# Optimization experiments

Measured on AMD Instinct MI355X. Metric: run time of the kernel, lower is better.

Reference implementation:

```python
import jax, jax.numpy as jnp
import numpy as np

D_MODEL = 768
D_STATE = 16
D_CONV = 4
EXPAND = 2
D_IN = D_MODEL // 2          # per-direction model dim = 384
D_INNER = EXPAND * D_IN      # ssm inner dim = 768
DT_RANK = (D_IN + 15) // 16  # 24 (mamba 'auto')
B, L = 2, 2048
EPS = 1e-5


def silu(x):
    return x * jax.nn.sigmoid(x)


def layernorm(x, w, b):
    m = jnp.mean(x, axis=-1, keepdims=True)
    v = jnp.var(x, axis=-1, keepdims=True)
    return (x - m) * jax.lax.rsqrt(v + EPS) * w + b


def causal_conv1d(u, w, b):
    # u: (B,L,di), w: (di,K) depthwise causal conv, b: (di,)
    K = w.shape[1]
    up = jnp.pad(u, ((0, 0), (K - 1, 0), (0, 0)))
    Lq = u.shape[1]
    y = sum(up[:, k:k + Lq, :] * w[:, k] for k in range(K))
    return y + b


def mamba_ssm(u, in_w, in_b, conv_w, conv_b, xp_w, dt_w, dt_b, A_log, Dp, out_w, out_b):
    # u: (B,L,D_IN)
    Bz = u.shape[0]
    xz = u @ in_w + in_b                         # (B,L,2*D_INNER)
    x, z = jnp.split(xz, 2, axis=-1)             # (B,L,D_INNER) each
    x = silu(causal_conv1d(x, conv_w, conv_b))
    xd = x @ xp_w                                # (B,L,DT_RANK+2N)
    dt = jax.nn.softplus(xd[..., :DT_RANK] @ dt_w + dt_b)   # (B,L,D_INNER)
    Bm = xd[..., DT_RANK:DT_RANK + D_STATE]      # (B,L,N)
    Cm = xd[..., DT_RANK + D_STATE:]             # (B,L,N)
    A = -jnp.exp(A_log)                          # (D_INNER,N)

    def step(h, xs):
        dt_t, x_t, B_t, C_t = xs                 # (B,di),(B,di),(B,N),(B,N)
        h = jnp.exp(dt_t[..., None] * A) * h + (dt_t * x_t)[..., None] * B_t[:, None, :]
        y = jnp.einsum('bdn,bn->bd', h, C_t)
        return h, y

    h0 = jnp.zeros((Bz, D_INNER, D_STATE), x.dtype)
    xs = (dt.transpose(1, 0, 2), x.transpose(1, 0, 2),
          Bm.transpose(1, 0, 2), Cm.transpose(1, 0, 2))
    _, ys = jax.lax.scan(step, h0, xs)           # ys: (L,B,D_INNER)
    y = ys.transpose(1, 0, 2) + x * Dp
    y = y * silu(z)
    return y @ out_w + out_b                     # (B,L,D_IN)


def setup_inputs() -> dict:
    key = jax.random.key(0)

    def nrm(i, shape, s=0.02):
        return jax.random.normal(jax.random.fold_in(key, i), shape, jnp.float32) * s

    d = {"x": jax.random.normal(jax.random.fold_in(key, 0), (B, L, D_MODEL), jnp.float32)}
    d["in_norm_w"] = jnp.ones(D_MODEL); d["in_norm_b"] = jnp.zeros(D_MODEL)
    d["ip_w"] = nrm(1, (D_MODEL, 2 * D_IN)); d["ip_b"] = jnp.zeros(2 * D_IN)
    i = 10
    for p in ("f", "b"):
        d[p + "_in_w"] = nrm(i, (D_IN, 2 * D_INNER)); d[p + "_in_b"] = jnp.zeros(2 * D_INNER)
        d[p + "_conv_w"] = nrm(i + 1, (D_INNER, D_CONV), 0.2); d[p + "_conv_b"] = jnp.zeros(D_INNER)
        d[p + "_xp_w"] = nrm(i + 2, (D_INNER, DT_RANK + 2 * D_STATE))
        d[p + "_dt_w"] = nrm(i + 3, (DT_RANK, D_INNER), 0.1)
        d[p + "_dt_b"] = nrm(i + 4, (D_INNER,), 0.5)
        d[p + "_A_log"] = jnp.log(jnp.tile(jnp.arange(1, D_STATE + 1, dtype=jnp.float32), (D_INNER, 1)))
        d[p + "_D"] = jnp.ones(D_INNER)
        d[p + "_out_w"] = nrm(i + 5, (D_INNER, D_IN)); d[p + "_out_b"] = jnp.zeros(D_IN)
        i += 10
    d["op_w"] = nrm(30, (2 * D_IN, D_MODEL)); d["op_b"] = jnp.zeros(D_MODEL)
    d["norm_w"] = jnp.ones(D_MODEL); d["norm_b"] = jnp.zeros(D_MODEL)
    return d


def reference(x, in_norm_w, in_norm_b, ip_w, ip_b,
              f_in_w, f_in_b, f_conv_w, f_conv_b, f_xp_w, f_dt_w, f_dt_b, f_A_log, f_D, f_out_w, f_out_b,
              b_in_w, b_in_b, b_conv_w, b_conv_b, b_xp_w, b_dt_w, b_dt_b, b_A_log, b_D, b_out_w, b_out_b,
              op_w, op_b, norm_w, norm_b):
    residual = x
    xn = layernorm(x, in_norm_w, in_norm_b)
    xp = xn @ ip_w + ip_b                        # (B,L,2*D_IN)
    x_fwd, x_bwd = jnp.split(xp, 2, axis=-1)
    out_fwd = mamba_ssm(x_fwd, f_in_w, f_in_b, f_conv_w, f_conv_b, f_xp_w,
                        f_dt_w, f_dt_b, f_A_log, f_D, f_out_w, f_out_b)
    out_bwd = mamba_ssm(jnp.flip(x_bwd, axis=1), b_in_w, b_in_b, b_conv_w, b_conv_b, b_xp_w,
                        b_dt_w, b_dt_b, b_A_log, b_D, b_out_w, b_out_b)
    out_bwd = jnp.flip(out_bwd, axis=1)
    out = jnp.concatenate([out_fwd, out_bwd], axis=-1) @ op_w + op_b
    # dropout is identity in eval mode
    return layernorm(residual + out, norm_w, norm_b)
```

## Files before the change

kernel.cpp:

```cpp
#include <hip/hip_runtime.h>
#include <hip/hip_bf16.h>
#include <math.h>
#include <type_traits>

#define BATCH 2
#define SEQ   2048
#define DMODEL 768
#define DIN   384
#define DINNER 768
#define DSTATE 16
#define DTRANK 24
#define ROWS  (BATCH*SEQ)
#define NCH   64
#define CLEN  (SEQ/NCH)

using short8  = __attribute__((ext_vector_type(8))) short;
using floatx4 = __attribute__((ext_vector_type(4))) float;

__device__ __forceinline__ ushort f2bf(float f) {
    union { float f; uint u; } v; v.f = f;
    uint r = (v.u + 0x7fffu + ((v.u >> 16) & 1u)) >> 16;
    return (ushort)r;
}
__device__ __forceinline__ float bf2f(ushort h) {
    union { uint u; float f; } v; v.u = ((uint)h) << 16;
    return v.f;
}
__device__ __forceinline__ void async16(const ushort* g, ushort* l) {
    __builtin_amdgcn_global_load_lds(
        (const __attribute__((address_space(1))) void*)g,
        (__attribute__((address_space(3))) void*)l,
        16, 0, 0);
}
__device__ __forceinline__ float softplus_fast(float v) {
    if (v > 20.f) return v;
    float e = __expf(-fabsf(v));
    return fmaxf(v, 0.f) + __logf(1.f + e);
}

template<int TM, int TN> struct GemmShT { ushort lA[TM * 64]; ushort lB[TN * 64]; };

template<int TM, int TN>
__device__ __forceinline__ void gemm_accum(
    const ushort* __restrict__ A, int lda,
    const ushort* __restrict__ Bt, int ldb,
    int K, int m0, int n0, GemmShT<TM, TN>& sh,
    floatx4 (&acc)[TM / 32][TN / 32])
{
    constexpr int WM = TM / 2, WN = TN / 2;
    constexpr int MT = WM / 16, NT = WN / 16;
    constexpr int AI = TM / 32, BI = TN / 32;
    const int tid = threadIdx.x;
    const int wave = tid >> 6, lane = tid & 63;
    const int wm = wave >> 1, wn = wave & 1;
    const int quad = lane >> 4, l16 = lane & 15;
    const int lrow = lane >> 3;
    const int lcol = ((lane & 7) ^ (lane >> 3)) * 8;

    for (int k0 = 0; k0 < K; k0 += 64) {
#pragma unroll
        for (int i = 0; i < AI; i++) {
            int rb = (wave * AI + i) * 8;
            async16(A + (size_t)(m0 + rb + lrow) * lda + k0 + lcol, &sh.lA[rb * 64]);
        }
#pragma unroll
        for (int i = 0; i < BI; i++) {
            int rb = (wave * BI + i) * 8;
            async16(Bt + (size_t)(n0 + rb + lrow) * ldb + k0 + lcol, &sh.lB[rb * 64]);
        }
        __syncthreads();
#pragma unroll
        for (int ks = 0; ks < 2; ks++) {
            short8 af[MT], bf[NT];
#pragma unroll
            for (int i = 0; i < MT; i++) {
                int row = wm * WM + i * 16 + l16;
                af[i] = *(const short8*)&sh.lA[row * 64 + ((ks * 4 + quad) ^ (row & 7)) * 8];
            }
#pragma unroll
            for (int j = 0; j < NT; j++) {
                int row = wn * WN + j * 16 + l16;
                bf[j] = *(const short8*)&sh.lB[row * 64 + ((ks * 4 + quad) ^ (row & 7)) * 8];
            }
#pragma unroll
            for (int i = 0; i < MT; i++)
#pragma unroll
                for (int j = 0; j < NT; j++)
                    acc[i][j] = __builtin_amdgcn_mfma_f32_16x16x32_bf16(af[i], bf[j], acc[i][j], 0, 0, 0);
        }
        __syncthreads();
    }
}

template<int TM, int TN, bool OUT_BF>
__device__ __forceinline__ void gemm_epilogue(
    const float* __restrict__ bias, void* __restrict__ C, int ldc, int N,
    int m0, int n0, floatx4 (&acc)[TM / 32][TN / 32])
{
    constexpr int WM = TM / 2, WN = TN / 2;
    constexpr int MT = WM / 16, NT = WN / 16;
    const int tid = threadIdx.x;
    const int wave = tid >> 6, lane = tid & 63;
    const int wm = wave >> 1, wn = wave & 1;
    const int quad = lane >> 4, l16 = lane & 15;
#pragma unroll
    for (int i = 0; i < MT; i++) {
#pragma unroll
        for (int j = 0; j < NT; j++) {
            int row = m0 + wm * WM + i * 16 + quad * 4;
            int col = n0 + wn * WN + j * 16 + l16;
            if (col < N) {
                float bv = bias ? bias[col] : 0.f;
#pragma unroll
                for (int r = 0; r < 4; r++) {
                    float v = acc[i][j][r] + bv;
                    if (OUT_BF) ((ushort*)C)[(size_t)(row + r) * ldc + col] = f2bf(v);
                    else        ((float*)C)[(size_t)(row + r) * ldc + col] = v;
                }
            }
        }
    }
}

template<int TM, int TN, bool OUT_BF>
__global__ __launch_bounds__(256) void mfma_gemm_k(
    const ushort* __restrict__ A0, const ushort* __restrict__ A1, int lda,
    const ushort* __restrict__ B0, const ushort* __restrict__ B1, int ldb,
    const float* __restrict__ bias0, const float* __restrict__ bias1,
    void* __restrict__ C0, void* __restrict__ C1, int ldc, int N, int K)
{
    __shared__ GemmShT<TM, TN> sh;
    const ushort* A  = blockIdx.z ? A1 : A0;
    const ushort* Bt = blockIdx.z ? B1 : B0;
    const float* bias = blockIdx.z ? bias1 : bias0;
    void* C = blockIdx.z ? C1 : C0;
    floatx4 acc[TM / 32][TN / 32];
#pragma unroll
    for (int i = 0; i < TM / 32; i++)
#pragma unroll
        for (int j = 0; j < TN / 32; j++)
            acc[i][j] = (floatx4){0.f, 0.f, 0.f, 0.f};
    int m0 = blockIdx.y * TM, n0 = blockIdx.x * TN;
    gemm_accum<TM, TN>(A, lda, Bt, ldb, K, m0, n0, sh, acc);
    gemm_epilogue<TM, TN, OUT_BF>(bias, C, ldc, N, m0, n0, acc);
}

__global__ __launch_bounds__(256) void dt_kernel(
    const ushort* __restrict__ xdf, const ushort* __restrict__ xdb,
    const ushort* __restrict__ dtwTf, const ushort* __restrict__ dtwTb,
    const float* __restrict__ dtbf, const float* __restrict__ dtbb,
    ushort* __restrict__ dtf, ushort* __restrict__ dtb)
{
    constexpr int TM = 128, TN = 64;
    __shared__ GemmShT<TM, TN> sh;
    const ushort* A  = blockIdx.z ? xdb : xdf;
    const ushort* Bt = blockIdx.z ? dtwTb : dtwTf;
    const float* bias = blockIdx.z ? dtbb : dtbf;
    ushort* C = blockIdx.z ? dtb : dtf;
    floatx4 acc[4][2];
#pragma unroll
    for (int i = 0; i < 4; i++)
#pragma unroll
        for (int j = 0; j < 2; j++)
            acc[i][j] = (floatx4){0.f, 0.f, 0.f, 0.f};
    int m0 = blockIdx.y * TM, n0 = blockIdx.x * TN;
    gemm_accum<TM, TN>(A, 64, Bt, 64, 64, m0, n0, sh, acc);
    const int tid = threadIdx.x;
    const int wave = tid >> 6, lane = tid & 63;
    const int wm = wave >> 1, wn = wave & 1;
    const int quad = lane >> 4, l16 = lane & 15;
#pragma unroll
    for (int i = 0; i < 4; i++) {
#pragma unroll
        for (int j = 0; j < 2; j++) {
            int row = m0 + wm * 64 + i * 16 + quad * 4;
            int col = n0 + wn * 32 + j * 16 + l16;
            float bv = bias[col];
#pragma unroll
            for (int r = 0; r < 4; r++)
                C[(size_t)(row + r) * 768 + col] = f2bf(softplus_fast(acc[i][j][r] + bv));
        }
    }
}

template<int TM, int TN>
__global__ __launch_bounds__(256) void outop_kernel(
    const ushort* __restrict__ A0, const ushort* __restrict__ B0,
    const ushort* __restrict__ A1, const ushort* __restrict__ B1,
    const float* __restrict__ bias, float* __restrict__ C,
    int lda, int ldb, int ldc, int N, int K)
{
    __shared__ GemmShT<TM, TN> sh;
    floatx4 acc[TM / 32][TN / 32];
#pragma unroll
    for (int i = 0; i < TM / 32; i++)
#pragma unroll
        for (int j = 0; j < TN / 32; j++)
            acc[i][j] = (floatx4){0.f, 0.f, 0.f, 0.f};
    int m0 = blockIdx.y * TM, n0 = blockIdx.x * TN;
    gemm_accum<TM, TN>(A0, lda, B0, ldb, K, m0, n0, sh, acc);
    gemm_accum<TM, TN>(A1, lda, B1, ldb, K, m0, n0, sh, acc);
    gemm_epilogue<TM, TN, false>(bias, (void*)C, ldc, N, m0, n0, acc);
}

struct LnSh { float ss[4]; float ssq[4]; float m; float rs; };

template<bool OUT_BF>
__device__ __forceinline__ void ln_row(
    int row, const float* __restrict__ x, const float* __restrict__ res,
    const float* __restrict__ w, const float* __restrict__ b,
    void* __restrict__ out, LnSh& sh)
{
    int tid = threadIdx.x;
    const float* xr = x + (size_t)row * DMODEL;
    const float* rr = res ? res + (size_t)row * DMODEL : nullptr;
    float v[3];
    float s = 0.f, sq = 0.f;
#pragma unroll
    for (int j = 0; j < 3; j++) {
        int i = tid + j * 256;
        float val = xr[i];
        if (rr) val += rr[i];
        v[j] = val; s += val; sq += val * val;
    }
#pragma unroll
    for (int off = 32; off; off >>= 1) {
        s  += __shfl_down(s,  off);
        sq += __shfl_down(sq, off);
    }
    int wid = tid >> 6;
    if ((tid & 63) == 0) { sh.ss[wid] = s; sh.ssq[wid] = sq; }
    __syncthreads();
    if (tid == 0) {
        float S  = sh.ss[0] + sh.ss[1] + sh.ss[2] + sh.ss[3];
        float SQ = sh.ssq[0] + sh.ssq[1] + sh.ssq[2] + sh.ssq[3];
        float m  = S * (1.0f / DMODEL);
        float var = SQ * (1.0f / DMODEL) - m * m;
        sh.m = m;
        sh.rs = rsqrtf(var + 1e-5f);
    }
    __syncthreads();
    float m = sh.m, rs = sh.rs;
#pragma unroll
    for (int j = 0; j < 3; j++) {
        int i = tid + j * 256;
        float r = (v[j] - m) * rs * w[i] + b[i];
        if (OUT_BF) ((ushort*)out)[(size_t)row * DMODEL + i] = f2bf(r);
        else        ((float*)out)[(size_t)row * DMODEL + i] = r;
    }
}

__global__ __launch_bounds__(256) void ln2_kernel(
    const float* __restrict__ x, const float* __restrict__ res,
    const float* __restrict__ w, const float* __restrict__ b,
    float* __restrict__ out)
{
    __shared__ LnSh sh;
    ln_row<false>(blockIdx.x, x, res, w, b, (void*)out, sh);
}

struct TD { const float* src; ushort* dst; int K, N, Kp, Np, ldd, tile0, tkp, mode; };
struct PrepArgs {
    TD d[12];
    int ntc;
    const float *x, *in_nw, *in_nb;
    ushort* xn;
};

__global__ __launch_bounds__(256) void prep_kernel(PrepArgs p)
{
    __shared__ union { float tile[32][33]; LnSh l; } sh;
    int bi = blockIdx.x;
    if (bi < p.ntc) {
        int i = 0;
        while (i < 11 && bi >= p.d[i + 1].tile0) i++;
        TD t = p.d[i];
        int local = bi - t.tile0;
        int tki = local % t.tkp, tn = local / t.tkp;
        int k0 = tki * 32, n0 = tn * 32;
        if (t.mode == 0) {
            int tx = threadIdx.x & 31, ty = threadIdx.x >> 5;
#pragma unroll
            for (int r = ty; r < 32; r += 8) {
                int k = k0 + r, n = n0 + tx;
                sh.tile[r][tx] = (k < t.K && n < t.N) ? t.src[(size_t)k * t.N + n] : 0.f;
            }
            __syncthreads();
#pragma unroll
            for (int r = ty; r < 32; r += 8) {
                int n = n0 + r, k = k0 + tx;
                t.dst[(size_t)n * t.ldd + k] = f2bf(sh.tile[tx][r]);
            }
        } else {
#pragma unroll
            for (int e = threadIdx.x; e < 1024; e += 256) {
                int r = e >> 5, c = e & 31;
                int k = k0 + r, n = n0 + c;
                float v = (k < t.K && n < t.N) ? t.src[(size_t)k * t.N + n] : 0.f;
                t.dst[(size_t)k * t.ldd + n] = f2bf(v);
            }
        }
    } else {
        ln_row<true>(bi - p.ntc, p.x, (const float*)nullptr, p.in_nw, p.in_nb,
                     (void*)p.xn, sh.l);
    }
}

struct WfArgs {
    const ushort *fin, *bin, *opT, *ipc, *fow, *bow;
    ushort *WzF, *WzB, *WoF, *WoB;
    const float *ip_b, *f_in_b, *b_in_b, *f_out_b, *b_out_b, *op_b;
    const float *f_in_w32, *b_in_w32, *op_w32;
    float *bzf, *bzb, *bo;
};

__global__ __launch_bounds__(256) void wfuse_kernel(WfArgs p)
{
    __shared__ GemmShT<128, 64> sh;
    int t = blockIdx.x;
    if (t < 6) {
        int n = t * 256 + threadIdx.x;
        float acc = p.f_in_b[n];
#pragma unroll 16
        for (int j = 0; j < 384; j++)
            acc = fmaf(p.ip_b[j], p.f_in_w32[(size_t)j * 1536 + n], acc);
        p.bzf[n] = acc;
    } else if (t < 12) {
        int n = (t - 6) * 256 + threadIdx.x;
        float acc = p.b_in_b[n];
#pragma unroll 16
        for (int j = 0; j < 384; j++)
            acc = fmaf(p.ip_b[384 + j], p.b_in_w32[(size_t)j * 1536 + n], acc);
        p.bzb[n] = acc;
    } else if (t < 15) {
        int n = (t - 12) * 256 + threadIdx.x;
        float acc = p.op_b[n];
#pragma unroll 16
        for (int j = 0; j < 384; j++)
            acc = fmaf(p.f_out_b[j], p.op_w32[(size_t)j * 768 + n], acc);
#pragma unroll 16
        for (int j = 0; j < 384; j++)
            acc = fmaf(p.b_out_b[j], p.op_w32[(size_t)(384 + j) * 768 + n], acc);
        p.bo[n] = acc;
    } else {
        int g = t - 15;
        const ushort *A, *Bt; ushort* C; int lda, ldb, m0, n0;
        if (g < 144)      { A = p.fin;       lda = 384; Bt = p.ipc;       ldb = 768; C = p.WzF; int u = g;       m0 = (u / 12) * 128; n0 = (u % 12) * 64; }
        else if (g < 288) { A = p.bin;       lda = 384; Bt = p.ipc + 384; ldb = 768; C = p.WzB; int u = g - 144; m0 = (u / 12) * 128; n0 = (u % 12) * 64; }
        else if (g < 360) { A = p.opT;       lda = 768; Bt = p.fow;       ldb = 384; C = p.WoF; int u = g - 288; m0 = (u / 12) * 128; n0 = (u % 12) * 64; }
        else              { A = p.opT + 384; lda = 768; Bt = p.bow;       ldb = 384; C = p.WoB; int u = g - 360; m0 = (u / 12) * 128; n0 = (u % 12) * 64; }
        floatx4 acc[4][2];
#pragma unroll
        for (int i = 0; i < 4; i++)
#pragma unroll
            for (int j = 0; j < 2; j++)
                acc[i][j] = (floatx4){0.f, 0.f, 0.f, 0.f};
        gemm_accum<128, 64>(A, lda, Bt, ldb, 384, m0, n0, sh, acc);
        gemm_epilogue<128, 64, true>((const float*)nullptr, (void*)C, 768, 768, m0, n0, acc);
    }
}

__global__ __launch_bounds__(256) void conv_silu_kernel(
    const ushort* __restrict__ xzf, const ushort* __restrict__ xzb,
    const float* __restrict__ cwf, const float* __restrict__ cbf,
    const float* __restrict__ cwb, const float* __restrict__ cbb,
    ushort* __restrict__ outf, ushort* __restrict__ outb)
{
    int rev = blockIdx.y;
    const ushort* xz = rev ? xzb : xzf;
    const float* cw = rev ? cwb : cwf;
    const float* cb = rev ? cbb : cbf;
    ushort* out = rev ? outb : outf;

    int idx = blockIdx.x * 256 + threadIdx.x;
    int d = idx % DINNER;
    int row = idx / DINNER;
    int t = row & (SEQ - 1), b = row >> 11;
    float4 w4 = *(const float4*)&cw[d * 4];
    float wk[4] = {w4.x, w4.y, w4.z, w4.w};
    float acc = cb[d];
#pragma unroll
    for (int k = 0; k < 4; k++) {
        int ts = rev ? (t + 3 - k) : (t - 3 + k);
        if (ts >= 0 && ts < SEQ)
            acc = fmaf(wk[k], bf2f(xz[((size_t)(b * SEQ + ts)) * 1536 + d]), acc);
    }
    float sig = 1.f / (1.f + __expf(-acc));
    out[idx] = f2bf(acc * sig);
}

template<bool FULL>
__global__ __launch_bounds__(256) void scan_chunk_kernel(
    const ushort* __restrict__ dtf, const ushort* __restrict__ xcf,
    const ushort* __restrict__ xdf, const ushort* __restrict__ xzf,
    const float* __restrict__ Alf, const float* __restrict__ Dff,
    const ushort* __restrict__ dtb, const ushort* __restrict__ xcb,
    const ushort* __restrict__ xdb, const ushort* __restrict__ xzb,
    const float* __restrict__ Alb, const float* __restrict__ Dbb,
    float* __restrict__ Hloc, float* __restrict__ Wp,
    const float* __restrict__ Hin,
    ushort* __restrict__ yf, ushort* __restrict__ yb)
{
    const int d     = blockIdx.x * 256 + threadIdx.x;
    const int chunk = blockIdx.y;
    const int bz    = blockIdx.z;
    const int dir   = bz >> 1;
    const int bat   = bz & 1;

    const ushort* dt = dir ? dtb : dtf;
    const ushort* xc = dir ? xcb : xcf;
    const ushort* xd = dir ? xdb : xdf;
    const ushort* xz = dir ? xzb : xzf;
    const float*  Al = dir ? Alb : Alf;
    const float*  Dp = dir ? Dbb : Dff;
    ushort* yo = dir ? yb : yf;

    float a[16];
    {
        const float4* Ap = (const float4*)(Al + (size_t)d * 16);
#pragma unroll
        for (int q = 0; q < 4; q++) {
            float4 v = Ap[q];
            a[q*4+0] = -__expf(v.x); a[q*4+1] = -__expf(v.y);
            a[q*4+2] = -__expf(v.z); a[q*4+3] = -__expf(v.w);
        }
    }
    const float a0 = a[0];
    bool fast = true;
#pragma unroll
    for (int n = 0; n < 16; n++) {
        float ideal = a0 * (float)(n + 1);
        fast = fast && (fabsf(a[n] - ideal) <= 1e-4f * fabsf(ideal) + 1e-7f);
    }

    float h[16];
    if (FULL) {
        size_t base = ((size_t)(bz * NCH + chunk) * DINNER + d) * 16;
#pragma unroll
        for (int q = 0; q < 4; q++) {
            float4 v = *(const float4*)(Hin + base + q * 4);
            h[q*4+0] = v.x; h[q*4+1] = v.y; h[q*4+2] = v.z; h[q*4+3] = v.w;
        }
    } else {
#pragma unroll
        for (int n = 0; n < 16; n++) h[n] = 0.f;
    }

    const float Dd = FULL ? Dp[d] : 0.f;
    float S = 0.f;

    auto run = [&](auto FASTC) {
        constexpr bool FAST = decltype(FASTC)::value;
#pragma unroll 2
        for (int i = 0; i < CLEN; i++) {
            int tl = chunk * CLEN + i;
            int t  = dir ? (SEQ - 1 - tl) : tl;
            size_t r = (size_t)(bat * SEQ + t);
            float dtv = bf2f(dt[r * DINNER + d]);
            float xv  = bf2f(xc[r * DINNER + d]);
            const ushort* bp = xd + r * 64 + DTRANK;
            short8 b0 = *(const short8*)(bp);
            short8 b1 = *(const short8*)(bp + 8);
            float Bv[16];
#pragma unroll
            for (int n = 0; n < 8; n++) {
                Bv[n]     = bf2f((ushort)b0[n]);
                Bv[8 + n] = bf2f((ushort)b1[n]);
            }
            float w[16];
            if (FAST) {
                float e1 = __expf(dtv * a0);
                float e2 = e1*e1, e4 = e2*e2, e8 = e4*e4;
                w[0]=e1;      w[1]=e2;      w[2]=e2*e1;   w[3]=e4;
                w[4]=e4*e1;   w[5]=e4*e2;   w[6]=e4*w[2]; w[7]=e8;
                w[8]=e8*e1;   w[9]=e8*e2;   w[10]=e8*w[2];w[11]=e8*e4;
                w[12]=e8*w[4];w[13]=e8*w[5];w[14]=e8*w[6];w[15]=e8*e8;
            } else {
#pragma unroll
                for (int n = 0; n < 16; n++) w[n] = __expf(dtv * a[n]);
            }
            float bx = dtv * xv;
#pragma unroll
            for (int n = 0; n < 16; n++)
                h[n] = fmaf(w[n], h[n], bx * Bv[n]);
            S += dtv;
            if (FULL) {
                short8 c0 = *(const short8*)(bp + 16);
                short8 c1 = *(const short8*)(bp + 24);
                float Cv[16];
#pragma unroll
                for (int n = 0; n < 8; n++) {
                    Cv[n]     = bf2f((ushort)c0[n]);
                    Cv[8 + n] = bf2f((ushort)c1[n]);
                }
                float y = 0.f;
#pragma unroll
                for (int n = 0; n < 16; n++) y = fmaf(h[n], Cv[n], y);
                float zv = bf2f(xz[r * 1536 + DINNER + d]);
                float sig = 1.f / (1.f + __expf(-zv));
                yo[r * DINNER + d] = f2bf((y + xv * Dd) * (zv * sig));
            }
        }
    };
    if (fast) run(std::true_type{}); else run(std::false_type{});

    if (!FULL) {
        float W[16];
        if (fast) {
            float E1 = __expf(S * a0);
            float E2 = E1*E1, E4 = E2*E2, E8 = E4*E4;
            W[0]=E1;      W[1]=E2;      W[2]=E2*E1;   W[3]=E4;
            W[4]=E4*E1;   W[5]=E4*E2;   W[6]=E4*W[2]; W[7]=E8;
            W[8]=E8*E1;   W[9]=E8*E2;   W[10]=E8*W[2];W[11]=E8*E4;
            W[12]=E8*W[4];W[13]=E8*W[5];W[14]=E8*W[6];W[15]=E8*E8;
        } else {
#pragma unroll
            for (int n = 0; n < 16; n++) W[n] = __expf(S * a[n]);
        }
        size_t base = ((size_t)(bz * NCH + chunk) * DINNER + d) * 16;
#pragma unroll
        for (int q = 0; q < 4; q++) {
            *(float4*)(Hloc + base + q*4) = make_float4(h[q*4+0], h[q*4+1], h[q*4+2], h[q*4+3]);
            *(float4*)(Wp   + base + q*4) = make_float4(W[q*4+0], W[q*4+1], W[q*4+2], W[q*4+3]);
        }
    }
}

__global__ __launch_bounds__(256) void scan_combine(
    const float* __restrict__ Hloc, const float* __restrict__ Wp,
    float* __restrict__ Hin)
{
    int idx = blockIdx.x * 256 + threadIdx.x;
    int bz = idx / (DINNER * 16);
    int rest = idx % (DINNER * 16);
    float hin = 0.f;
#pragma unroll 4
    for (int k = 0; k < NCH; k++) {
        size_t o = (size_t)(bz * NCH + k) * (DINNER * 16) + rest;
        Hin[o] = hin;
        hin = fmaf(Wp[o], hin, Hloc[o]);
    }
}

extern "C" void kernel_launch(void* const* d_in, const int* in_sizes, int n_in,
                              void* d_out, int out_size, void* d_ws, size_t ws_size,
                              hipStream_t stream)
{
    const float* x        = (const float*)d_in[0];
    const float* in_nw    = (const float*)d_in[1];
    const float* in_nb    = (const float*)d_in[2];
    const float* ip_w     = (const float*)d_in[3];
    const float* ip_b     = (const float*)d_in[4];
    const float* f_in_w   = (const float*)d_in[5];
    const float* f_in_b   = (const float*)d_in[6];
    const float* f_conv_w = (const float*)d_in[7];
    const float* f_conv_b = (const float*)d_in[8];
    const float* f_xp_w   = (const float*)d_in[9];
    const float* f_dt_w   = (const float*)d_in[10];
    const float* f_dt_b   = (const float*)d_in[11];
    const float* f_A_log  = (const float*)d_in[12];
    const float* f_D      = (const float*)d_in[13];
    const float* f_out_w  = (const float*)d_in[14];
    const float* f_out_b  = (const float*)d_in[15];
    const float* b_in_w   = (const float*)d_in[16];
    const float* b_in_b   = (const float*)d_in[17];
    const float* b_conv_w = (const float*)d_in[18];
    const float* b_conv_b = (const float*)d_in[19];
    const float* b_xp_w   = (const float*)d_in[20];
    const float* b_dt_w   = (const float*)d_in[21];
    const float* b_dt_b   = (const float*)d_in[22];
    const float* b_A_log  = (const float*)d_in[23];
    const float* b_D      = (const float*)d_in[24];
    const float* b_out_w  = (const float*)d_in[25];
    const float* b_out_b  = (const float*)d_in[26];
    const float* op_w     = (const float*)d_in[27];
    const float* op_b     = (const float*)d_in[28];
    const float* norm_w   = (const float*)d_in[29];
    const float* norm_b   = (const float*)d_in[30];

    size_t off = 0;
    auto alloc = [&](size_t bytes) {
        void* p = (char*)d_ws + off;
        off += (bytes + 255) & ~(size_t)255;
        return p;
    };
    const size_t R = ROWS;
    ushort* xn_bf   = (ushort*)alloc(R * 768 * 2);
    ushort* xz_f_bf = (ushort*)alloc(R * 1536 * 2);
    ushort* xz_b_bf = (ushort*)alloc(R * 1536 * 2);
    ushort* xc_f_bf = (ushort*)alloc(R * 768 * 2);
    ushort* xc_b_bf = (ushort*)alloc(R * 768 * 2);
    ushort* xd64_f  = (ushort*)alloc(R * 64 * 2);
    ushort* xd64_b  = (ushort*)alloc(R * 64 * 2);
    ushort* dt_f    = (ushort*)alloc(R * 768 * 2);
    ushort* dt_b    = (ushort*)alloc(R * 768 * 2);
    ushort* y_f_bf  = (ushort*)alloc(R * 768 * 2);
    ushort* y_b_bf  = (ushort*)alloc(R * 768 * 2);
    float*  outraw  = (float*)alloc(R * 768 * 4);
    const size_t SCN = (size_t)4 * NCH * DINNER * 16;
    float* Hloc = (float*)alloc(SCN * 4);
    float* Wpb  = (float*)alloc(SCN * 4);
    float* Hin  = (float*)alloc(SCN * 4);
    ushort* Wt_fin = (ushort*)alloc((size_t)1536 * 384 * 2);
    ushort* Wt_bin = (ushort*)alloc((size_t)1536 * 384 * 2);
    ushort* Wt_op  = (ushort*)alloc((size_t)768 * 768 * 2);
    ushort* Wt_fxp = (ushort*)alloc((size_t)64 * 768 * 2);
    ushort* Wt_bxp = (ushort*)alloc((size_t)64 * 768 * 2);
    ushort* dtwT_f = (ushort*)alloc((size_t)768 * 64 * 2);
    ushort* dtwT_b = (ushort*)alloc((size_t)768 * 64 * 2);
    ushort* ipc    = (ushort*)alloc((size_t)768 * 768 * 2);
    ushort* fow    = (ushort*)alloc((size_t)768 * 384 * 2);
    ushort* bow    = (ushort*)alloc((size_t)768 * 384 * 2);
    ushort* WzF    = (ushort*)alloc((size_t)1536 * 768 * 2);
    ushort* WzB    = (ushort*)alloc((size_t)1536 * 768 * 2);
    ushort* WoF    = (ushort*)alloc((size_t)768 * 768 * 2);
    ushort* WoB    = (ushort*)alloc((size_t)768 * 768 * 2);
    float*  bzf    = (float*)alloc(1536 * 4);
    float*  bzb    = (float*)alloc(1536 * 4);
    float*  bo     = (float*)alloc(768 * 4);

    PrepArgs pa;
    int tile0 = 0, nd = 0;
    auto add = [&](const float* s, ushort* dst, int K, int N, int Kp, int Np,
                   int ldd, int mode) {
        pa.d[nd] = TD{s, dst, K, N, Kp, Np, ldd, tile0, Kp / 32, mode};
        tile0 += (Kp / 32) * (Np / 32);
        nd++;
    };
    add(f_in_w,  Wt_fin, 384, 1536, 384, 1536, 384, 0);
    add(b_in_w,  Wt_bin, 384, 1536, 384, 1536, 384, 0);
    add(op_w,    Wt_op,  768, 768,  768, 768,  768, 0);
    add(f_xp_w,  Wt_fxp, 768, 56,   768, 64,   768, 0);
    add(b_xp_w,  Wt_bxp, 768, 56,   768, 64,   768, 0);
    add(f_dt_w,  dtwT_f, 24,  768,  64,  768,  64,  0);
    add(b_dt_w,  dtwT_b, 24,  768,  64,  768,  64,  0);
    add(ip_w,    ipc,    768, 768,  768, 768,  768, 1);
    add(f_out_w, fow,    768, 384,  768, 384,  384, 1);
    add(b_out_w, bow,    768, 384,  768, 384,  384, 1);
    pa.ntc = tile0;
    for (int i = nd; i < 12; i++) pa.d[i].tile0 = 0x7fffffff;
    pa.x = x; pa.in_nw = in_nw; pa.in_nb = in_nb; pa.xn = xn_bf;
    hipLaunchKernelGGL(prep_kernel, dim3(tile0 + ROWS), dim3(256), 0, stream, pa);

    WfArgs wa;
    wa.fin = Wt_fin; wa.bin = Wt_bin; wa.opT = Wt_op;
    wa.ipc = ipc; wa.fow = fow; wa.bow = bow;
    wa.WzF = WzF; wa.WzB = WzB; wa.WoF = WoF; wa.WoB = WoB;
    wa.ip_b = ip_b; wa.f_in_b = f_in_b; wa.b_in_b = b_in_b;
    wa.f_out_b = f_out_b; wa.b_out_b = b_out_b; wa.op_b = op_b;
    wa.f_in_w32 = f_in_w; wa.b_in_w32 = b_in_w; wa.op_w32 = op_w;
    wa.bzf = bzf; wa.bzb = bzb; wa.bo = bo;
    hipLaunchKernelGGL(wfuse_kernel, dim3(447), dim3(256), 0, stream, wa);

    hipLaunchKernelGGL((mfma_gemm_k<128, 128, true>), dim3(12, 32, 2), dim3(256), 0, stream,
                       xn_bf, xn_bf, 768, WzF, WzB, 768, bzf, bzb,
                       (void*)xz_f_bf, (void*)xz_b_bf, 1536, 1536, 768);

    hipLaunchKernelGGL(conv_silu_kernel, dim3(ROWS * DINNER / 256, 2), dim3(256), 0, stream,
                       xz_f_bf, xz_b_bf, f_conv_w, f_conv_b, b_conv_w, b_conv_b,
                       xc_f_bf, xc_b_bf);

    hipLaunchKernelGGL((mfma_gemm_k<64, 64, true>), dim3(1, 64, 2), dim3(256), 0, stream,
                       xc_f_bf, xc_b_bf, 768, Wt_fxp, Wt_bxp, 768,
                       (const float*)nullptr, (const float*)nullptr,
                       (void*)xd64_f, (void*)xd64_b, 64, 64, 768);

    hipLaunchKernelGGL(dt_kernel, dim3(12, 32, 2), dim3(256), 0, stream,
                       xd64_f, xd64_b, dtwT_f, dtwT_b, f_dt_b, b_dt_b, dt_f, dt_b);

    hipLaunchKernelGGL((scan_chunk_kernel<false>), dim3(DINNER / 256, NCH, 4), dim3(256), 0, stream,
                       dt_f, xc_f_bf, xd64_f, xz_f_bf, f_A_log, f_D,
                       dt_b, xc_b_bf, xd64_b, xz_b_bf, b_A_log, b_D,
                       Hloc, Wpb, (const float*)nullptr, (ushort*)nullptr, (ushort*)nullptr);
    hipLaunchKernelGGL(scan_combine, dim3(4 * DINNER * 16 / 256), dim3(256), 0, stream,
                       Hloc, Wpb, Hin);
    hipLaunchKernelGGL((scan_chunk_kernel<true>), dim3(DINNER / 256, NCH, 4), dim3(256), 0, stream,
                       dt_f, xc_f_bf, xd64_f, xz_f_bf, f_A_log, f_D,
                       dt_b, xc_b_bf, xd64_b, xz_b_bf, b_A_log, b_D,
                       (float*)nullptr, (float*)nullptr, Hin, y_f_bf, y_b_bf);

    hipLaunchKernelGGL((outop_kernel<128, 64>), dim3(12, 32), dim3(256), 0, stream,
                       y_f_bf, WoF, y_b_bf, WoB, bo, outraw, 768, 768, 768, 768, 768);

    hipLaunchKernelGGL(ln2_kernel, dim3(ROWS), dim3(256), 0, stream,
                       x, outraw, norm_w, norm_b, (float*)d_out);
}
```

Measured before the change: 324.1 us.

## Fuse conv+SiLU into x_proj/dt GEMM and recompute conv inside scan

Removes the standalone conv_silu kernel and the xc intermediate buffers. A new xddt kernel computes the causal conv and SiLU on the fly while staging the A tile for the x_proj GEMM, then reuses the xd tile in LDS to compute the dt projection with softplus. The scan kernels recompute conv+SiLU from xz using a sliding register window instead of reading xc. This saves two launches and the xc write/read traffic, at the cost of redundant conv work in the scan passes and a less parallel xddt grid (128 blocks).

```diff
diff --git a/kernel.cpp b/kernel.cpp
--- a/kernel.cpp
+++ b/kernel.cpp
@@ -145,41 +145,159 @@
     gemm_epilogue<TM, TN, OUT_BF>(bias, C, ldc, N, m0, n0, acc);
 }
 
-__global__ __launch_bounds__(256) void dt_kernel(
-    const ushort* __restrict__ xdf, const ushort* __restrict__ xdb,
+__global__ __launch_bounds__(256) void xddt_kernel(
+    const ushort* __restrict__ xzf, const ushort* __restrict__ xzb,
+    const float* __restrict__ cwf, const float* __restrict__ cbf,
+    const float* __restrict__ cwb, const float* __restrict__ cbb,
+    const ushort* __restrict__ WxpF, const ushort* __restrict__ WxpB,
     const ushort* __restrict__ dtwTf, const ushort* __restrict__ dtwTb,
     const float* __restrict__ dtbf, const float* __restrict__ dtbb,
+    ushort* __restrict__ xdf, ushort* __restrict__ xdb,
     ushort* __restrict__ dtf, ushort* __restrict__ dtb)
 {
-    constexpr int TM = 128, TN = 64;
-    __shared__ GemmShT<TM, TN> sh;
-    const ushort* A  = blockIdx.z ? xdb : xdf;
-    const ushort* Bt = blockIdx.z ? dtwTb : dtwTf;
-    const float* bias = blockIdx.z ? dtbb : dtbf;
-    ushort* C = blockIdx.z ? dtb : dtf;
-    floatx4 acc[4][2];
-#pragma unroll
-    for (int i = 0; i < 4; i++)
-#pragma unroll
-        for (int j = 0; j < 2; j++)
-            acc[i][j] = (floatx4){0.f, 0.f, 0.f, 0.f};
-    int m0 = blockIdx.y * TM, n0 = blockIdx.x * TN;
-    gemm_accum<TM, TN>(A, 64, Bt, 64, 64, m0, n0, sh, acc);
+    __shared__ ushort lA[64 * 64];
+    __shared__ ushort lB[64 * 64];
+    const int dir = blockIdx.z;
+    const ushort* xz = dir ? xzb : xzf;
+    const float* cw = dir ? cwb : cwf;
+    const float* cb = dir ? cbb : cbf;
+    const ushort* Wxp  = dir ? WxpB : WxpF;
+    const ushort* dtwT = dir ? dtwTb : dtwTf;
+    const float* dtbias = dir ? dtbb : dtbf;
+    ushort* xd = dir ? xdb : xdf;
+    ushort* dt = dir ? dtb : dtf;
+    const int m0 = blockIdx.y * 64;
     const int tid = threadIdx.x;
     const int wave = tid >> 6, lane = tid & 63;
     const int wm = wave >> 1, wn = wave & 1;
     const int quad = lane >> 4, l16 = lane & 15;
-#pragma unroll
-    for (int i = 0; i < 4; i++) {
+    const int lrow = lane >> 3, lcol = ((lane & 7) ^ (lane >> 3)) * 8;
+
+    floatx4 acc[2][2];
+#pragma unroll
+    for (int i = 0; i < 2; i++)
+#pragma unroll
+        for (int j = 0; j < 2; j++)
+            acc[i][j] = (floatx4){0.f, 0.f, 0.f, 0.f};
+
+    for (int k0 = 0; k0 < 768; k0 += 64) {
+#pragma unroll
+        for (int c = 0; c < 2; c++) {
+            int flat = tid + c * 256;
+            int row = flat >> 3, colg = flat & 7;
+            int r = m0 + row, b = r >> 11, t = r & (SEQ - 1);
+            int d0 = k0 + colg * 8;
+            float a8[8];
+#pragma unroll
+            for (int cc = 0; cc < 8; cc++) a8[cc] = cb[d0 + cc];
+#pragma unroll
+            for (int kk = 0; kk < 4; kk++) {
+                int ts = dir ? (t + 3 - kk) : (t - 3 + kk);
+                if (ts >= 0 && ts < SEQ) {
+                    short8 v = *(const short8*)&xz[((size_t)(b * SEQ + ts)) * 1536 + d0];
+#pragma unroll
+                    for (int cc = 0; cc < 8; cc++)
+                        a8[cc] = fmaf(cw[(d0 + cc) * 4 + kk], bf2f((ushort)v[cc]), a8[cc]);
+                }
+            }
+            short8 o;
+#pragma unroll
+            for (int cc = 0; cc < 8; cc++) {
+                float sig = 1.f / (1.f + __expf(-a8[cc]));
+                o[cc] = (short)f2bf(a8[cc] * sig);
+            }
+            *(short8*)&lA[row * 64 + ((colg ^ (row & 7)) * 8)] = o;
+        }
+#pragma unroll
+        for (int i = 0; i < 2; i++) {
+            int rb = (wave * 2 + i) * 8;
+            async16(Wxp + (size_t)(rb + lrow) * 768 + k0 + lcol, &lB[rb * 64]);
+        }
+        __syncthreads();
+#pragma unroll
+        for (int ks = 0; ks < 2; ks++) {
+            short8 af[2], bfr[2];
+#pragma unroll
+            for (int i = 0; i < 2; i++) {
+                int row = wm * 32 + i * 16 + l16;
+                af[i] = *(const short8*)&lA[row * 64 + ((ks * 4 + quad) ^ (row & 7)) * 8];
+            }
+#pragma unroll
+            for (int j = 0; j < 2; j++) {
+                int row = wn * 32 + j * 16 + l16;
+                bfr[j] = *(const short8*)&lB[row * 64 + ((ks * 4 + quad) ^ (row & 7)) * 8];
+            }
+#pragma unroll
+            for (int i = 0; i < 2; i++)
+#pragma unroll
+                for (int j = 0; j < 2; j++)
+                    acc[i][j] = __builtin_amdgcn_mfma_f32_16x16x32_bf16(af[i], bfr[j], acc[i][j], 0, 0, 0);
+        }
+        __syncthreads();
+    }
+
+#pragma unroll
+    for (int i = 0; i < 2; i++) {
 #pragma unroll
         for (int j = 0; j < 2; j++) {
-            int row = m0 + wm * 64 + i * 16 + quad * 4;
-            int col = n0 + wn * 32 + j * 16 + l16;
-            float bv = bias[col];
-#pragma unroll
-            for (int r = 0; r < 4; r++)
-                C[(size_t)(row + r) * 768 + col] = f2bf(softplus_fast(acc[i][j][r] + bv));
-        }
+            int lr0 = wm * 32 + i * 16 + quad * 4;
+            int col = wn * 32 + j * 16 + l16;
+#pragma unroll
+            for (int r = 0; r < 4; r++) {
+                int lr = lr0 + r;
+                ushort hv = f2bf(acc[i][j][r]);
+                xd[(size_t)(m0 + lr) * 64 + col] = hv;
+                lA[lr * 64 + ((col >> 3) ^ (lr & 7)) * 8 + (col & 7)] = hv;
+            }
+        }
+    }
+    __syncthreads();
+
+    for (int nt = 0; nt < 12; nt++) {
+#pragma unroll
+        for (int i = 0; i < 2; i++) {
+            int rb = (wave * 2 + i) * 8;
+            async16(dtwT + (size_t)(nt * 64 + rb + lrow) * 64 + lcol, &lB[rb * 64]);
+        }
+        __syncthreads();
+        floatx4 a2[2][2];
+#pragma unroll
+        for (int i = 0; i < 2; i++)
+#pragma unroll
+            for (int j = 0; j < 2; j++)
+                a2[i][j] = (floatx4){0.f, 0.f, 0.f, 0.f};
+#pragma unroll
+        for (int ks = 0; ks < 2; ks++) {
+            short8 af[2], bfr[2];
+#pragma unroll
+            for (int i = 0; i < 2; i++) {
+                int row = wm * 32 + i * 16 + l16;
+                af[i] = *(const short8*)&lA[row * 64 + ((ks * 4 + quad) ^ (row & 7)) * 8];
+            }
+#pragma unroll
+            for (int j = 0; j < 2; j++) {
+                int row = wn * 32 + j * 16 + l16;
+                bfr[j] = *(const short8*)&lB[row * 64 + ((ks * 4 + quad) ^ (row & 7)) * 8];
+            }
+#pragma unroll
+            for (int i = 0; i < 2; i++)
+#pragma unroll
+                for (int j = 0; j < 2; j++)
+                    a2[i][j] = __builtin_amdgcn_mfma_f32_16x16x32_bf16(af[i], bfr[j], a2[i][j], 0, 0, 0);
+        }
+#pragma unroll
+        for (int i = 0; i < 2; i++) {
+#pragma unroll
+            for (int j = 0; j < 2; j++) {
+                int row = m0 + wm * 32 + i * 16 + quad * 4;
+                int col = nt * 64 + wn * 32 + j * 16 + l16;
+                float bv = dtbias[col];
+#pragma unroll
+                for (int r = 0; r < 4; r++)
+                    dt[(size_t)(row + r) * 768 + col] = f2bf(softplus_fast(a2[i][j][r] + bv));
+            }
+        }
+        __syncthreads();
     }
 }
 
@@ -360,42 +478,15 @@
     }
 }
 
-__global__ __launch_bounds__(256) void conv_silu_kernel(
-    const ushort* __restrict__ xzf, const ushort* __restrict__ xzb,
-    const float* __restrict__ cwf, const float* __restrict__ cbf,
-    const float* __restrict__ cwb, const float* __restrict__ cbb,
-    ushort* __restrict__ outf, ushort* __restrict__ outb)
-{
-    int rev = blockIdx.y;
-    const ushort* xz = rev ? xzb : xzf;
-    const float* cw = rev ? cwb : cwf;
-    const float* cb = rev ? cbb : cbf;
-    ushort* out = rev ? outb : outf;
-
-    int idx = blockIdx.x * 256 + threadIdx.x;
-    int d = idx % DINNER;
-    int row = idx / DINNER;
-    int t = row & (SEQ - 1), b = row >> 11;
-    float4 w4 = *(const float4*)&cw[d * 4];
-    float wk[4] = {w4.x, w4.y, w4.z, w4.w};
-    float acc = cb[d];
-#pragma unroll
-    for (int k = 0; k < 4; k++) {
-        int ts = rev ? (t + 3 - k) : (t - 3 + k);
-        if (ts >= 0 && ts < SEQ)
-            acc = fmaf(wk[k], bf2f(xz[((size_t)(b * SEQ + ts)) * 1536 + d]), acc);
-    }
-    float sig = 1.f / (1.f + __expf(-acc));
-    out[idx] = f2bf(acc * sig);
-}
-
 template<bool FULL>
 __global__ __launch_bounds__(256) void scan_chunk_kernel(
-    const ushort* __restrict__ dtf, const ushort* __restrict__ xcf,
-    const ushort* __restrict__ xdf, const ushort* __restrict__ xzf,
+    const ushort* __restrict__ dtf, const ushort* __restrict__ xdf,
+    const ushort* __restrict__ xzf,
+    const float* __restrict__ cwf, const float* __restrict__ cbf,
     const float* __restrict__ Alf, const float* __restrict__ Dff,
-    const ushort* __restrict__ dtb, const ushort* __restrict__ xcb,
-    const ushort* __restrict__ xdb, const ushort* __restrict__ xzb,
+    const ushort* __restrict__ dtb, const ushort* __restrict__ xdb,
+    const ushort* __restrict__ xzb,
+    const float* __restrict__ cwb, const float* __restrict__ cbb,
     const float* __restrict__ Alb, const float* __restrict__ Dbb,
     float* __restrict__ Hloc, float* __restrict__ Wp,
     const float* __restrict__ Hin,
@@ -408,9 +499,10 @@
     const int bat   = bz & 1;
 
     const ushort* dt = dir ? dtb : dtf;
-    const ushort* xc = dir ? xcb : xcf;
     const ushort* xd = dir ? xdb : xdf;
     const ushort* xz = dir ? xzb : xzf;
+    const float*  cw = dir ? cwb : cwf;
+    const float*  cb = dir ? cbb : cbf;
     const float*  Al = dir ? Alb : Alf;
     const float*  Dp = dir ? Dbb : Dff;
     ushort* yo = dir ? yb : yf;
@@ -447,7 +539,20 @@
     }
 
     const float Dd = FULL ? Dp[d] : 0.f;
+    const float4 w4 = *(const float4*)&cw[d * 4];
+    const float cbd = cb[d];
     float S = 0.f;
+
+    float win0, win1, win2;
+    {
+        int t0 = dir ? (SEQ - 1 - chunk * CLEN) : chunk * CLEN;
+        auto ldu = [&](int ts) -> float {
+            return (ts >= 0 && ts < SEQ)
+                ? bf2f(xz[((size_t)(bat * SEQ + ts)) * 1536 + d]) : 0.f;
+        };
+        if (!dir) { win0 = ldu(t0 - 3); win1 = ldu(t0 - 2); win2 = ldu(t0 - 1); }
+        else      { win0 = ldu(t0 + 3); win1 = ldu(t0 + 2); win2 = ldu(t0 + 1); }
+    }
 
     auto run = [&](auto FASTC) {
         constexpr bool FAST = decltype(FASTC)::value;
@@ -457,7 +562,16 @@
             int t  = dir ? (SEQ - 1 - tl) : tl;
             size_t r = (size_t)(bat * SEQ + t);
             float dtv = bf2f(dt[r * DINNER + d]);
-            float xv  = bf2f(xc[r * DINNER + d]);
+            float cur = bf2f(xz[r * 1536 + d]);
+            float cv = cbd;
+            cv = fmaf(w4.x, win0, cv);
+            cv = fmaf(w4.y, win1, cv);
+            cv = fmaf(w4.z, win2, cv);
+            cv = fmaf(w4.w, cur, cv);
+            win0 = win1; win1 = win2; win2 = cur;
+            float csig = 1.f / (1.f + __expf(-cv));
+            float xv = cv * csig;
+
             const ushort* bp = xd + r * 64 + DTRANK;
             short8 b0 = *(const short8*)(bp);
             short8 b1 = *(const short8*)(bp + 8);
@@ -588,8 +702,6 @@
     ushort* xn_bf   = (ushort*)alloc(R * 768 * 2);
     ushort* xz_f_bf = (ushort*)alloc(R * 1536 * 2);
     ushort* xz_b_bf = (ushort*)alloc(R * 1536 * 2);
-    ushort* xc_f_bf = (ushort*)alloc(R * 768 * 2);
-    ushort* xc_b_bf = (ushort*)alloc(R * 768 * 2);
     ushort* xd64_f  = (ushort*)alloc(R * 64 * 2);
     ushort* xd64_b  = (ushort*)alloc(R * 64 * 2);
     ushort* dt_f    = (ushort*)alloc(R * 768 * 2);
@@ -656,27 +768,20 @@
                        xn_bf, xn_bf, 768, WzF, WzB, 768, bzf, bzb,
                        (void*)xz_f_bf, (void*)xz_b_bf, 1536, 1536, 768);
 
-    hipLaunchKernelGGL(conv_silu_kernel, dim3(ROWS * DINNER / 256, 2), dim3(256), 0, stream,
+    hipLaunchKernelGGL(xddt_kernel, dim3(1, ROWS / 64, 2), dim3(256), 0, stream,
                        xz_f_bf, xz_b_bf, f_conv_w, f_conv_b, b_conv_w, b_conv_b,
-                       xc_f_bf, xc_b_bf);
-
-    hipLaunchKernelGGL((mfma_gemm_k<64, 64, true>), dim3(1, 64, 2), dim3(256), 0, stream,
-                       xc_f_bf, xc_b_bf, 768, Wt_fxp, Wt_bxp, 768,
-                       (const float*)nullptr, (const float*)nullptr,
-                       (void*)xd64_f, (void*)xd64_b, 64, 64, 768);
-
-    hipLaunchKernelGGL(dt_kernel, dim3(12, 32, 2), dim3(256), 0, stream,
-                       xd64_f, xd64_b, dtwT_f, dtwT_b, f_dt_b, b_dt_b, dt_f, dt_b);
+                       Wt_fxp, Wt_bxp, dtwT_f, dtwT_b, f_dt_b, b_dt_b,
+                       xd64_f, xd64_b, dt_f, dt_b);
 
     hipLaunchKernelGGL((scan_chunk_kernel<false>), dim3(DINNER / 256, NCH, 4), dim3(256), 0, stream,
-                       dt_f, xc_f_bf, xd64_f, xz_f_bf, f_A_log, f_D,
-                       dt_b, xc_b_bf, xd64_b, xz_b_bf, b_A_log, b_D,
+                       dt_f, xd64_f, xz_f_bf, f_conv_w, f_conv_b, f_A_log, f_D,
+                       dt_b, xd64_b, xz_b_bf, b_conv_w, b_conv_b, b_A_log, b_D,
                        Hloc, Wpb, (const float*)nullptr, (ushort*)nullptr, (ushort*)nullptr);
     hipLaunchKernelGGL(scan_combine, dim3(4 * DINNER * 16 / 256), dim3(256), 0, stream,
                        Hloc, Wpb, Hin);
     hipLaunchKernelGGL((scan_chunk_kernel<true>), dim3(DINNER / 256, NCH, 4), dim3(256), 0, stream,
-                       dt_f, xc_f_bf, xd64_f, xz_f_bf, f_A_log, f_D,
-                       dt_b, xc_b_bf, xd64_b, xz_b_bf, b_A_log, b_D,
+                       dt_f, xd64_f, xz_f_bf, f_conv_w, f_conv_b, f_A_log, f_D,
+                       dt_b, xd64_b, xz_b_bf, b_conv_w, b_conv_b, b_A_log, b_D,
                        (float*)nullptr, (float*)nullptr, Hin, y_f_bf, y_b_bf);
 
     hipLaunchKernelGGL((outop_kernel<128, 64>), dim3(12, 32), dim3(256), 0, stream,
```

Result: slower. 382.7 us (+18.1%).
